# Kernel tuning notes

Measured on AMD Instinct MI355X. Metric: run time of the kernel, lower is better.

## Reference

```python
import jax, jax.numpy as jnp
import numpy as np

N_NODES = 100000
N_EDGES = 1600000
IN_F = 128
HEADS = 4
D_K = 32
OUT_TOTAL = HEADS * D_K


def setup_inputs() -> dict:
    key = jax.random.key(0)
    k1, k2, k3, k4, k5, k6 = jax.random.split(key, 6)
    x = jax.random.normal(k1, (N_NODES, IN_F), dtype=jnp.float32)
    edge_index = jax.random.randint(k2, (2, N_EDGES), 0, N_NODES, dtype=jnp.int64)
    # torch nn.Linear weights: [out, in], xavier-uniform init
    def xavier(k, shape):
        fan_out, fan_in = shape
        lim = float(np.sqrt(6.0 / (fan_in + fan_out)))
        return jax.random.uniform(k, shape, dtype=jnp.float32, minval=-lim, maxval=lim)
    Wq = xavier(k3, (OUT_TOTAL, IN_F))
    Wk = xavier(k4, (OUT_TOTAL, IN_F))
    Wv = xavier(k5, (OUT_TOTAL, IN_F))
    # D init_type='uniform': U(-1, 1)
    D = jax.random.uniform(k6, (HEADS, D_K), dtype=jnp.float32, minval=-1.0, maxval=1.0)
    return {"x": x, "Wq": Wq, "Wk": Wk, "Wv": Wv, "D": D, "edge_index": edge_index}


def reference(x, Wq, Wk, Wv, D, edge_index):
    N = x.shape[0]
    scale = 1.0 / np.sqrt(D_K)
    Q = (x @ Wq.T).reshape(N, HEADS, D_K)
    K = (x @ Wk.T).reshape(N, HEADS, D_K)
    V = (x @ Wv.T).reshape(N, HEADS, D_K)
    row, col = edge_index[0], edge_index[1]
    K_i = K[row]              # [E, H, d]
    Q_j = Q[col]              # [E, H, d]
    diff = K_i - Q_j
    # non-self edges: diff^T diag(D) diff ; self edges: K^T diag(D) Q
    score_edge = jnp.sum(diff * D * diff, axis=-1)          # [E, H]
    score_self = jnp.sum(K_i * D * Q[row], axis=-1)         # [E, H]
    self_mask = (row == col)[:, None]
    scores = jnp.where(self_mask, score_self, score_edge)
    scores = jax.nn.leaky_relu(scores * scale, 0.2)
    # segment softmax over destination node `row`
    smax = jax.ops.segment_max(scores, row, num_segments=N)  # [N, H]
    ex = jnp.exp(scores - smax[row])
    ssum = jax.ops.segment_sum(ex, row, num_segments=N)      # [N, H]
    alpha = ex / (ssum[row] + 1e-16)
    # scatter-add aggregate alpha * V[col] into destination rows
    out = jax.ops.segment_sum(alpha[:, :, None] * V[col], row, num_segments=N)
    return out.reshape(N, OUT_TOTAL)
```

## Files before the change

### kernel.cpp

```cpp
#include <hip/hip_runtime.h>
#include <hip/hip_fp16.h>
#include <cmath>


#define HEADS 4
#define DK 32
#define FDIM 128

typedef _Float16 f16x8 __attribute__((ext_vector_type(8)));
typedef float f32x4 __attribute__((ext_vector_type(4)));

__global__ __launch_bounds__(256) void init_buffers(
    int* __restrict__ cursor, int n)
{
    int gid = blockIdx.x * 256 + threadIdx.x;
    if (gid < n) cursor[gid] = 0;
}

__device__ __forceinline__ int swz_idx(int row, int kk) {
    return (row * FDIM + kk) ^ ((row & 7) << 3);
}

__device__ __forceinline__ void stage_w(
    const float* __restrict__ src, _Float16* __restrict__ dst,
    int tid, bool lo)
{
    const int kk0 = (tid & 15) * 8;
    const int r0  = tid >> 4;
#pragma unroll
    for (int i = 0; i < 8; ++i) {
        const int row = i * 16 + r0;
        const float* p = src + (size_t)row * FDIM + kk0;
        float4 v0 = *reinterpret_cast<const float4*>(p);
        float4 v1 = *reinterpret_cast<const float4*>(p + 4);
        const float vv[8] = {v0.x, v0.y, v0.z, v0.w, v1.x, v1.y, v1.z, v1.w};
        f16x8 h;
#pragma unroll
        for (int j = 0; j < 8; ++j) {
            _Float16 hh = (_Float16)vv[j];
            h[j] = lo ? (_Float16)(vv[j] - (float)hh) : hh;
        }
        *reinterpret_cast<f16x8*>(&dst[swz_idx(row, kk0)]) = h;
    }
}

__device__ __forceinline__ void stage_x(
    const float* __restrict__ src, _Float16* __restrict__ dh,
    _Float16* __restrict__ dl, int n0, int nmax, int tid)
{
    const int kk0 = (tid & 15) * 8;
    const int r0  = tid >> 4;
#pragma unroll
    for (int i = 0; i < 4; ++i) {
        const int row = i * 16 + r0;
        float4 v0 = make_float4(0.f, 0.f, 0.f, 0.f), v1 = v0;
        if (n0 + row < nmax) {
            const float* p = src + (size_t)(n0 + row) * FDIM + kk0;
            v0 = *reinterpret_cast<const float4*>(p);
            v1 = *reinterpret_cast<const float4*>(p + 4);
        }
        const float vv[8] = {v0.x, v0.y, v0.z, v0.w, v1.x, v1.y, v1.z, v1.w};
        f16x8 h, l;
#pragma unroll
        for (int j = 0; j < 8; ++j) {
            _Float16 hh = (_Float16)vv[j];
            h[j] = hh;
            l[j] = (_Float16)(vv[j] - (float)hh);
        }
        const int si = swz_idx(row, kk0);
        *reinterpret_cast<f16x8*>(&dh[si]) = h;
        *reinterpret_cast<f16x8*>(&dl[si]) = l;
    }
}

__device__ __forceinline__ void mm_tile(
    const _Float16* __restrict__ xs, const _Float16* __restrict__ ws,
    f32x4 (&acc)[2][4], int lane, int wr0, int wc0)
{
    const int lrow = lane & 15;
    const int lk   = (lane >> 4) * 8;
#pragma unroll
    for (int kc = 0; kc < 4; ++kc) {
        f16x8 af[2], bf[4];
#pragma unroll
        for (int a = 0; a < 2; ++a)
            af[a] = *reinterpret_cast<const f16x8*>(
                &xs[swz_idx(wr0 + a * 16 + lrow, kc * 32 + lk)]);
#pragma unroll
        for (int b = 0; b < 4; ++b)
            bf[b] = *reinterpret_cast<const f16x8*>(
                &ws[swz_idx(wc0 + b * 16 + lrow, kc * 32 + lk)]);
#pragma unroll
        for (int a = 0; a < 2; ++a)
#pragma unroll
            for (int b = 0; b < 4; ++b)
                acc[a][b] = __builtin_amdgcn_mfma_f32_16x16x32_f16(
                    af[a], bf[b], acc[a][b], 0, 0, 0);
    }
}

__global__ __launch_bounds__(256) void qkv_and_fill(
    const float* __restrict__ x, const float* __restrict__ Wq,
    const float* __restrict__ Wk, const float* __restrict__ Wv,
    __half* __restrict__ QVh, float* __restrict__ Kout, int N, int NQ,
    const int* __restrict__ row, const int* __restrict__ col,
    int* __restrict__ cursor, int* __restrict__ csr, int E)
{
    __shared__ __align__(16) _Float16 xh[64 * 128];
    __shared__ __align__(16) _Float16 xl[64 * 128];
    __shared__ __align__(16) _Float16 ws[128 * 128];

    if (blockIdx.x >= NQ) {
        const int t  = (blockIdx.x - NQ) * 256 + threadIdx.x;
        const int e0 = t * 4;
        if (e0 + 3 < E) {
            const int4 r4 = *reinterpret_cast<const int4*>(row + e0);
            const int4 c4 = *reinterpret_cast<const int4*>(col + e0);
            const int rr[4] = {r4.x, r4.y, r4.z, r4.w};
            const int cc[4] = {c4.x, c4.y, c4.z, c4.w};
#pragma unroll
            for (int k = 0; k < 4; ++k) {
                const int r = rr[k];
                if ((unsigned)r < (unsigned)N) {
                    const int p = atomicAdd(&cursor[r], 1);
                    if (p < 64) csr[(r << 6) + p] = cc[k];
                }
            }
        } else {
            for (int e = e0; e < E; ++e) {
                const int r = row[e];
                if ((unsigned)r < (unsigned)N) {
                    const int p = atomicAdd(&cursor[r], 1);
                    if (p < 64) csr[(r << 6) + p] = col[e];
                }
            }
        }
        return;
    }

    const int n0  = blockIdx.x * 64;
    const int tid = threadIdx.x;
    const int lane = tid & 63;
    const int wv   = tid >> 6;
    const int wr0  = (wv >> 1) * 32;
    const int wc0  = (wv & 1) * 64;
    const int orow = (lane >> 4) * 4;
    const int ocol = lane & 15;

    const float* Wp[3] = {Wq, Wk, Wv};

    stage_x(x, xh, xl, n0, N, tid);

    for (int p = 0; p < 3; ++p) {
        f32x4 acc[2][4];
#pragma unroll
        for (int a = 0; a < 2; ++a)
#pragma unroll
            for (int b = 0; b < 4; ++b)
                acc[a][b] = (f32x4){0.f, 0.f, 0.f, 0.f};

        stage_w(Wp[p], ws, tid, false);
        __syncthreads();
        mm_tile(xh, ws, acc, lane, wr0, wc0);
        mm_tile(xl, ws, acc, lane, wr0, wc0);
        __syncthreads();
        stage_w(Wp[p], ws, tid, true);
        __syncthreads();
        mm_tile(xh, ws, acc, lane, wr0, wc0);

        if (p == 1) {
#pragma unroll
            for (int a = 0; a < 2; ++a) {
#pragma unroll
                for (int r = 0; r < 4; ++r) {
                    const int n = n0 + wr0 + a * 16 + orow + r;
                    if (n < N) {
                        float* op = Kout + (size_t)n * FDIM + wc0 + ocol;
#pragma unroll
                        for (int b = 0; b < 4; ++b)
                            op[b * 16] = acc[a][b][r];
                    }
                }
            }
        } else {
            const int voff = (p == 2) ? 2 : 0;
#pragma unroll
            for (int a = 0; a < 2; ++a) {
#pragma unroll
                for (int r = 0; r < 4; ++r) {
                    const int n = n0 + wr0 + a * 16 + orow + r;
                    if (n < N) {
                        __half* op = QVh + (size_t)n * 256;
#pragma unroll
                        for (int b = 0; b < 4; ++b) {
                            const int d_o = wc0 + ocol + b * 16;
                            op[((d_o >> 1) << 2) + (d_o & 1) + voff] =
                                __float2half(acc[a][b][r]);
                        }
                    }
                }
            }
        }
        __syncthreads();
    }
}

__global__ __launch_bounds__(256) void fused_aggregate(
    const int* __restrict__ cursor, const int* __restrict__ csr,
    const __half* __restrict__ QVh, const float* Kb,
    const float* __restrict__ D, float* out, int N)
{
    int node = blockIdx.x * 4 + (threadIdx.x >> 6);
    if (node >= N) return;
    int lane = threadIdx.x & 63;
    int d = lane * 2;
    const float2 kv = *reinterpret_cast<const float2*>(Kb + (size_t)node * FDIM + d);
    const float D0 = D[d], D1 = D[d + 1];
    int cnt = cursor[node];
    cnt = (cnt < 64) ? cnt : 64;
    const int j0 = node << 6;
    float a0 = 0.0f, a1 = 0.0f, se = 0.0f;

    int cc0, cc1, cc2, cc3;
    float2 t0, t1, t2, t3;

    const int ec = (lane < cnt) ? csr[j0 + lane] : 0;

#define LOADF(s, idx) { int c_ = __shfl(ec, (idx)); cc##s = c_; \
    t##s = *reinterpret_cast<const float2*>( \
        reinterpret_cast<const __half*>(QVh) + (size_t)c_ * 256 + (lane << 2)); }

#define PROC(s) { \
    float2 qf = __half22float2(*reinterpret_cast<__half2*>(&t##s.x)); \
    float2 vf = __half22float2(*reinterpret_cast<__half2*>(&t##s.y)); \
    float p; \
    if (cc##s == node) { p = D0 * kv.x * qf.x + D1 * kv.y * qf.y; } \
    else { float dx = kv.x - qf.x, dy = kv.y - qf.y; \
           p = D0 * dx * dx + D1 * dy * dy; } \
    p += __shfl_xor(p, 1); p += __shfl_xor(p, 2); \
    p += __shfl_xor(p, 4); p += __shfl_xor(p, 8); \
    float z = p * 0.17677669529663687f; \
    z = fmaxf(z, 0.2f * z); \
    float ex = __expf(z); \
    a0 += ex * vf.x; a1 += ex * vf.y; se += ex; }

    int j = 0;
    if (cnt >= 4) {
        LOADF(0, 0) LOADF(1, 1) LOADF(2, 2) LOADF(3, 3)
        while (j + 8 <= cnt) {
            PROC(0) LOADF(0, j + 4)
            PROC(1) LOADF(1, j + 5)
            PROC(2) LOADF(2, j + 6)
            PROC(3) LOADF(3, j + 7)
            j += 4;
        }
        PROC(0) PROC(1) PROC(2) PROC(3)
        j += 4;
    }
    for (; j < cnt; ++j) {
        LOADF(0, j)
        PROC(0)
    }
#undef LOADF
#undef PROC

    float inv = 1.0f / (se + 1e-16f);
    *reinterpret_cast<float2*>(out + (size_t)node * FDIM + d) =
        make_float2(a0 * inv, a1 * inv);
}

extern "C" void kernel_launch(void* const* d_in, const int* in_sizes, int n_in,
                              void* d_out, int out_size, void* d_ws, size_t ws_size,
                              hipStream_t stream) {
    const float* x  = (const float*)d_in[0];
    const float* Wq = (const float*)d_in[1];
    const float* Wk = (const float*)d_in[2];
    const float* Wv = (const float*)d_in[3];
    const float* D  = (const float*)d_in[4];
    const int*  edge = (const int*)d_in[5];
    float* out = (float*)d_out;

    const int N = in_sizes[0] / FDIM;
    const int E = in_sizes[5] / 2;
    const int* row = edge;
    const int* col = edge + E;

    __half* QVh = (__half*)d_ws;
    int* cursor = (int*)(QVh + (size_t)N * 256);
    int* csr    = cursor + N;
    float* Kout = out;

    const int NQ = (N + 63) / 64;
    const int NF = (E + 1023) / 1024;

    init_buffers<<<(N + 255) / 256, 256, 0, stream>>>(cursor, N);

    qkv_and_fill<<<NQ + NF, 256, 0, stream>>>(
        x, Wq, Wk, Wv, QVh, Kout, N, NQ, row, col, cursor, csr, E);

    fused_aggregate<<<(N + 3) / 4, 256, 0, stream>>>(
        cursor, csr, QVh, Kout, D, out, N);
}
```

Before: 368.3 us.

## Pre-split weights into fp16 hi/lo fragments and read them directly from global memory

Adds a small kernel that converts Wq/Wk/Wv once into fp16 high and low parts stored in MFMA-fragment order. The GEMM kernel then loads weight fragments straight from global memory (L2-resident) instead of restaging and reconverting each weight into shared memory per block. This removes the block-level syncs and the 32KB weight LDS buffer, which may raise occupancy. The edge bucket fill is split out of the fused GEMM launch into its own kernel, trading the previous overlap within one launch for extra launches and sequential execution.

```diff
diff --git a/kernel.cpp b/kernel.cpp
--- a/kernel.cpp
+++ b/kernel.cpp
@@ -17,31 +17,70 @@
     if (gid < n) cursor[gid] = 0;
 }
 
+__global__ __launch_bounds__(256) void split_w(
+    const float* __restrict__ Wq, const float* __restrict__ Wk,
+    const float* __restrict__ Wv, _Float16* __restrict__ Whf,
+    _Float16* __restrict__ Wlf)
+{
+    const int p = blockIdx.x;
+    const float* __restrict__ W = (p == 0) ? Wq : (p == 1 ? Wk : Wv);
+#pragma unroll
+    for (int i = 0; i < 8; ++i) {
+        const int id = i * 256 + threadIdx.x;
+        const int g  = id >> 8;
+        const int kc = (id >> 6) & 3;
+        const int l  = id & 63;
+        const int row  = g * 16 + (l & 15);
+        const int col0 = kc * 32 + (l >> 4) * 8;
+        const float* src = W + row * FDIM + col0;
+        const float4 v0 = *reinterpret_cast<const float4*>(src);
+        const float4 v1 = *reinterpret_cast<const float4*>(src + 4);
+        const float vv[8] = {v0.x, v0.y, v0.z, v0.w, v1.x, v1.y, v1.z, v1.w};
+        f16x8 h, lo;
+#pragma unroll
+        for (int j = 0; j < 8; ++j) {
+            _Float16 hh = (_Float16)vv[j];
+            h[j]  = hh;
+            lo[j] = (_Float16)(vv[j] - (float)hh);
+        }
+        const size_t off = ((size_t)((p * 8 + g) * 4 + kc) * 64 + l) * 8;
+        *reinterpret_cast<f16x8*>(Whf + off) = h;
+        *reinterpret_cast<f16x8*>(Wlf + off) = lo;
+    }
+}
+
+__global__ __launch_bounds__(256) void fill_buckets(
+    const int* __restrict__ row, const int* __restrict__ col,
+    int* __restrict__ cursor, int* __restrict__ csr, int E, int N)
+{
+    const int t  = blockIdx.x * 256 + threadIdx.x;
+    const int e0 = t * 4;
+    if (e0 + 3 < E) {
+        const int4 r4 = *reinterpret_cast<const int4*>(row + e0);
+        const int4 c4 = *reinterpret_cast<const int4*>(col + e0);
+        const int rr[4] = {r4.x, r4.y, r4.z, r4.w};
+        const int cc[4] = {c4.x, c4.y, c4.z, c4.w};
+#pragma unroll
+        for (int k = 0; k < 4; ++k) {
+            const int r = rr[k];
+            if ((unsigned)r < (unsigned)N) {
+                const int p = atomicAdd(&cursor[r], 1);
+                if (p < 64) csr[(r << 6) + p] = cc[k];
+            }
+        }
+    } else {
+        for (int e = e0; e < E; ++e) {
+            const int r = row[e];
+            if ((unsigned)r < (unsigned)N) {
+                const int p = atomicAdd(&cursor[r], 1);
+                if (p < 64) csr[(r << 6) + p] = col[e];
+            }
+        }
+    }
+}
+
 __device__ __forceinline__ int swz_idx(int row, int kk) {
     return (row * FDIM + kk) ^ ((row & 7) << 3);
-}
-
-__device__ __forceinline__ void stage_w(
-    const float* __restrict__ src, _Float16* __restrict__ dst,
-    int tid, bool lo)
-{
-    const int kk0 = (tid & 15) * 8;
-    const int r0  = tid >> 4;
-#pragma unroll
-    for (int i = 0; i < 8; ++i) {
-        const int row = i * 16 + r0;
-        const float* p = src + (size_t)row * FDIM + kk0;
-        float4 v0 = *reinterpret_cast<const float4*>(p);
-        float4 v1 = *reinterpret_cast<const float4*>(p + 4);
-        const float vv[8] = {v0.x, v0.y, v0.z, v0.w, v1.x, v1.y, v1.z, v1.w};
-        f16x8 h;
-#pragma unroll
-        for (int j = 0; j < 8; ++j) {
-            _Float16 hh = (_Float16)vv[j];
-            h[j] = lo ? (_Float16)(vv[j] - (float)hh) : hh;
-        }
-        *reinterpret_cast<f16x8*>(&dst[swz_idx(row, kk0)]) = h;
-    }
 }
 
 __device__ __forceinline__ void stage_x(
@@ -73,70 +112,13 @@
     }
 }
 
-__device__ __forceinline__ void mm_tile(
-    const _Float16* __restrict__ xs, const _Float16* __restrict__ ws,
-    f32x4 (&acc)[2][4], int lane, int wr0, int wc0)
-{
-    const int lrow = lane & 15;
-    const int lk   = (lane >> 4) * 8;
-#pragma unroll
-    for (int kc = 0; kc < 4; ++kc) {
-        f16x8 af[2], bf[4];
-#pragma unroll
-        for (int a = 0; a < 2; ++a)
-            af[a] = *reinterpret_cast<const f16x8*>(
-                &xs[swz_idx(wr0 + a * 16 + lrow, kc * 32 + lk)]);
-#pragma unroll
-        for (int b = 0; b < 4; ++b)
-            bf[b] = *reinterpret_cast<const f16x8*>(
-                &ws[swz_idx(wc0 + b * 16 + lrow, kc * 32 + lk)]);
-#pragma unroll
-        for (int a = 0; a < 2; ++a)
-#pragma unroll
-            for (int b = 0; b < 4; ++b)
-                acc[a][b] = __builtin_amdgcn_mfma_f32_16x16x32_f16(
-                    af[a], bf[b], acc[a][b], 0, 0, 0);
-    }
-}
-
-__global__ __launch_bounds__(256) void qkv_and_fill(
-    const float* __restrict__ x, const float* __restrict__ Wq,
-    const float* __restrict__ Wk, const float* __restrict__ Wv,
-    __half* __restrict__ QVh, float* __restrict__ Kout, int N, int NQ,
-    const int* __restrict__ row, const int* __restrict__ col,
-    int* __restrict__ cursor, int* __restrict__ csr, int E)
+__global__ __launch_bounds__(256) void qkv_gemm(
+    const float* __restrict__ x, const _Float16* __restrict__ Whf,
+    const _Float16* __restrict__ Wlf, __half* __restrict__ QVh,
+    float* __restrict__ Kout, int N)
 {
     __shared__ __align__(16) _Float16 xh[64 * 128];
     __shared__ __align__(16) _Float16 xl[64 * 128];
-    __shared__ __align__(16) _Float16 ws[128 * 128];
-
-    if (blockIdx.x >= NQ) {
-        const int t  = (blockIdx.x - NQ) * 256 + threadIdx.x;
-        const int e0 = t * 4;
-        if (e0 + 3 < E) {
-            const int4 r4 = *reinterpret_cast<const int4*>(row + e0);
-            const int4 c4 = *reinterpret_cast<const int4*>(col + e0);
-            const int rr[4] = {r4.x, r4.y, r4.z, r4.w};
-            const int cc[4] = {c4.x, c4.y, c4.z, c4.w};
-#pragma unroll
-            for (int k = 0; k < 4; ++k) {
-                const int r = rr[k];
-                if ((unsigned)r < (unsigned)N) {
-                    const int p = atomicAdd(&cursor[r], 1);
-                    if (p < 64) csr[(r << 6) + p] = cc[k];
-                }
-            }
-        } else {
-            for (int e = e0; e < E; ++e) {
-                const int r = row[e];
-                if ((unsigned)r < (unsigned)N) {
-                    const int p = atomicAdd(&cursor[r], 1);
-                    if (p < 64) csr[(r << 6) + p] = col[e];
-                }
-            }
-        }
-        return;
-    }
 
     const int n0  = blockIdx.x * 64;
     const int tid = threadIdx.x;
@@ -144,12 +126,15 @@
     const int wv   = tid >> 6;
     const int wr0  = (wv >> 1) * 32;
     const int wc0  = (wv & 1) * 64;
+    const int g0   = wc0 >> 4;
     const int orow = (lane >> 4) * 4;
     const int ocol = lane & 15;
 
-    const float* Wp[3] = {Wq, Wk, Wv};
-
     stage_x(x, xh, xl, n0, N, tid);
+    __syncthreads();
+
+    const int lrow = lane & 15;
+    const int lk   = (lane >> 4) * 8;
 
     for (int p = 0; p < 3; ++p) {
         f32x4 acc[2][4];
@@ -159,14 +144,41 @@
             for (int b = 0; b < 4; ++b)
                 acc[a][b] = (f32x4){0.f, 0.f, 0.f, 0.f};
 
-        stage_w(Wp[p], ws, tid, false);
-        __syncthreads();
-        mm_tile(xh, ws, acc, lane, wr0, wc0);
-        mm_tile(xl, ws, acc, lane, wr0, wc0);
-        __syncthreads();
-        stage_w(Wp[p], ws, tid, true);
-        __syncthreads();
-        mm_tile(xh, ws, acc, lane, wr0, wc0);
+#pragma unroll
+        for (int kc = 0; kc < 4; ++kc) {
+            f16x8 afh[2], afl[2], bfh[4], bfl[4];
+#pragma unroll
+            for (int a = 0; a < 2; ++a) {
+                const int si = swz_idx(wr0 + a * 16 + lrow, kc * 32 + lk);
+                afh[a] = *reinterpret_cast<const f16x8*>(&xh[si]);
+                afl[a] = *reinterpret_cast<const f16x8*>(&xl[si]);
+            }
+#pragma unroll
+            for (int b = 0; b < 4; ++b) {
+                const size_t off =
+                    ((size_t)((p * 8 + g0 + b) * 4 + kc) * 64 + lane) * 8;
+                bfh[b] = *reinterpret_cast<const f16x8*>(Whf + off);
+                bfl[b] = *reinterpret_cast<const f16x8*>(Wlf + off);
+            }
+#pragma unroll
+            for (int a = 0; a < 2; ++a)
+#pragma unroll
+                for (int b = 0; b < 4; ++b)
+                    acc[a][b] = __builtin_amdgcn_mfma_f32_16x16x32_f16(
+                        afh[a], bfh[b], acc[a][b], 0, 0, 0);
+#pragma unroll
+            for (int a = 0; a < 2; ++a)
+#pragma unroll
+                for (int b = 0; b < 4; ++b)
+                    acc[a][b] = __builtin_amdgcn_mfma_f32_16x16x32_f16(
+                        afl[a], bfh[b], acc[a][b], 0, 0, 0);
+#pragma unroll
+            for (int a = 0; a < 2; ++a)
+#pragma unroll
+                for (int b = 0; b < 4; ++b)
+                    acc[a][b] = __builtin_amdgcn_mfma_f32_16x16x32_f16(
+                        afh[a], bfl[b], acc[a][b], 0, 0, 0);
+        }
 
         if (p == 1) {
 #pragma unroll
@@ -201,7 +213,6 @@
                 }
             }
         }
-        __syncthreads();
     }
 }
 
@@ -288,15 +299,18 @@
     __half* QVh = (__half*)d_ws;
     int* cursor = (int*)(QVh + (size_t)N * 256);
     int* csr    = cursor + N;
+    _Float16* Whf = (_Float16*)(csr + (size_t)N * 64);
+    _Float16* Wlf = Whf + 3 * 16384;
     float* Kout = out;
 
-    const int NQ = (N + 63) / 64;
-    const int NF = (E + 1023) / 1024;
-
     init_buffers<<<(N + 255) / 256, 256, 0, stream>>>(cursor, N);
-
-    qkv_and_fill<<<NQ + NF, 256, 0, stream>>>(
-        x, Wq, Wk, Wv, QVh, Kout, N, NQ, row, col, cursor, csr, E);
+    split_w<<<3, 256, 0, stream>>>(Wq, Wk, Wv, Whf, Wlf);
+
+    fill_buckets<<<(E + 1023) / 1024, 256, 0, stream>>>(
+        row, col, cursor, csr, E, N);
+
+    qkv_gemm<<<(N + 63) / 64, 256, 0, stream>>>(
+        x, Whf, Wlf, QVh, Kout, N);
 
     fused_aggregate<<<(N + 3) / 4, 256, 0, stream>>>(
         cursor, csr, QVh, Kout, D, out, N);
```

After: 428.4 us. +16.3%, slower.
